# Kernel tuning notes

Measured on AMD Instinct MI355X. Metric: run time of the kernel, lower is better.

The kernel has to match this reference:

```python
import jax, jax.numpy as jnp
import numpy as np
import math

B, M, H, K, SPAN = 8, 1024, 512, 8, 1024
D = H // K
MK = M + SPAN


def _skew(X, pad_value):
    # shift every row one step to the right: [N, M, L] -> [N, M, M+L]
    N, m, L = X.shape
    X = jnp.pad(X, ((0, 0), (0, 0), (0, m + 1)), constant_values=pad_value)
    X = X.reshape(N, -1)[:, :-m]
    return X.reshape(N, m, m + L)


def _unskew(X):
    # reverse of _skew: [N, M, M+L] -> [N, M, L]
    N, m, Lk = X.shape
    L = Lk - m
    X = jnp.pad(X.reshape(N, -1), ((0, 0), (0, m)))
    return X.reshape(N, m, Lk + 1)[:, :, :L]


def setup_inputs() -> dict:
    key0 = jax.random.key(0)
    ks = jax.random.split(key0, 8)
    w_scale = 1.0 / math.sqrt(H)
    return {
        "query": jax.random.normal(ks[0], (B, M, H), jnp.float32),
        "key": jax.random.normal(ks[1], (B, MK, H), jnp.float32),
        "value": jax.random.normal(ks[2], (B, MK, H), jnp.float32),
        "pos_encoding": jax.random.normal(ks[3], (D, SPAN), jnp.float32) * w_scale,
        "Wq": jax.random.normal(ks[4], (H, H), jnp.float32) * w_scale,
        "Wk": jax.random.normal(ks[5], (H, H), jnp.float32) * w_scale,
        "Wv": jax.random.normal(ks[6], (H, H), jnp.float32) * w_scale,
        "Wo": jax.random.normal(ks[7], (H, H), jnp.float32) * w_scale,
    }


def _heads(x, W):
    # project then split heads: [B, T, H] -> [B*K, T, D]
    x = x @ W
    Bx, T, _ = x.shape
    x = x.reshape(Bx, T, K, D).transpose(0, 2, 1, 3)
    return x.reshape(Bx * K, T, D)


def reference(query, key, value, pos_encoding, Wq, Wk, Wv, Wo):
    q = _heads(query, Wq)      # [B*K, M, D]
    k = _heads(key, Wk)        # [B*K, MK, D]
    v = _heads(value, Wv)      # [B*K, MK, D]

    attn_ctx = jnp.einsum("nmd,nld->nml", q, k)   # [B*K, M, MK]
    attn_ctx = _unskew(attn_ctx)                    # [B*K, M, SPAN]
    attn_pos = jnp.einsum("nmd,ds->nms", q, pos_encoding)  # [B*K, M, SPAN]
    attn = jax.nn.softmax((attn_ctx + attn_pos) / math.sqrt(D), axis=-1)

    attn_sk = _skew(attn, 0.0)                      # [B*K, M, MK]
    out = jnp.einsum("nml,nld->nmd", attn_sk, v)   # [B*K, M, D]
    out = out.reshape(B, K, M, D).transpose(0, 2, 1, 3).reshape(B, M, H)
    return out @ Wo
```

## Files before the change

### kernel.cpp

```cpp
#include <hip/hip_runtime.h>
#include <stdint.h>

#define Bq 8
#define Mq 1024
#define Hq 512
#define NHq 8
#define Dq 64
#define SPANq 1024
#define MKq 2048
#define PR2 168

typedef __bf16 bf16x8 __attribute__((ext_vector_type(8)));
typedef _Float16 f16x8 __attribute__((ext_vector_type(8)));
typedef float f32x4 __attribute__((ext_vector_type(4)));
typedef unsigned short ushort8 __attribute__((ext_vector_type(8)));
typedef unsigned int uint2v __attribute__((ext_vector_type(2)));

static __device__ __forceinline__ unsigned short f2bf(float f) {
  union { float f; unsigned u; } x; x.f = f;
  unsigned r = x.u + 0x7FFFu + ((x.u >> 16) & 1u);
  return (unsigned short)(r >> 16);
}

static __device__ __forceinline__ unsigned pk_f16(float a, float b) {
  return __builtin_bit_cast(unsigned, __builtin_amdgcn_cvt_pkrtz(a, b));
}

static __device__ __forceinline__ f32x4 mfma_bf16(bf16x8 a, bf16x8 b, f32x4 c) {
  return __builtin_amdgcn_mfma_f32_16x16x32_bf16(a, b, c, 0, 0, 0);
}
static __device__ __forceinline__ f32x4 mfma_f16(f16x8 a, f16x8 b, f32x4 c) {
  return __builtin_amdgcn_mfma_f32_16x16x32_f16(a, b, c, 0, 0, 0);
}

static __device__ __forceinline__ void async_ld16(const void* g, void* l) {
  __builtin_amdgcn_global_load_lds(
      (const __attribute__((address_space(1))) void*)g,
      (__attribute__((address_space(3))) void*)l, 16, 0, 0);
}

__global__ __launch_bounds__(256) void conv_bf16(
    const float* __restrict__ q, const float* __restrict__ k,
    const float* __restrict__ v, unsigned short* __restrict__ qo,
    unsigned short* __restrict__ ko, unsigned short* __restrict__ vo) {
  const int z = blockIdx.y;
  const float* src = (z == 0) ? q : (z == 1) ? k : v;
  unsigned short* dst = (z == 0) ? qo : (z == 1) ? ko : vo;
  const int n = (z == 0) ? (Bq * Mq * Hq) : (Bq * MKq * Hq);
  const int idx = (blockIdx.x * 256 + threadIdx.x) * 8;
  if (idx >= n) return;
  const f32x4 f0 = *(const f32x4*)(src + idx);
  const f32x4 f1 = *(const f32x4*)(src + idx + 4);
  ushort8 h;
  h[0] = f2bf(f0[0]); h[1] = f2bf(f0[1]); h[2] = f2bf(f0[2]); h[3] = f2bf(f0[3]);
  h[4] = f2bf(f1[0]); h[5] = f2bf(f1[1]); h[6] = f2bf(f1[2]); h[7] = f2bf(f1[3]);
  *(ushort8*)(dst + idx) = h;
}

__global__ __launch_bounds__(256) void prep_transpose(
    const float* __restrict__ Wq, const float* __restrict__ Wk,
    const float* __restrict__ Wv, const float* __restrict__ Wo,
    const float* __restrict__ pos,
    unsigned short* __restrict__ WTq, unsigned short* __restrict__ WTk,
    unsigned short* __restrict__ WTv, unsigned short* __restrict__ WTo,
    unsigned short* __restrict__ posT) {
  __shared__ float tile[64][65];
  const int bid = blockIdx.x;
  const float* src; unsigned short* dst;
  int src_stride, dst_stride, i0, o0;
  if (bid < 256) {
    const int w = bid >> 6, t = bid & 63;
    src = (w == 0) ? Wq : (w == 1) ? Wk : (w == 2) ? Wv : Wo;
    dst = (w == 0) ? WTq : (w == 1) ? WTk : (w == 2) ? WTv : WTo;
    src_stride = Hq; dst_stride = Hq;
    i0 = (t >> 3) * 64; o0 = (t & 7) * 64;
  } else {
    const int t = bid - 256;
    src = pos; dst = posT;
    src_stride = SPANq; dst_stride = Dq;
    i0 = 0; o0 = t * 64;
  }
  const int tid = threadIdx.x;
  for (int e = tid; e < 4096; e += 256) {
    const int r = e >> 6, c = e & 63;
    tile[r][c] = src[(size_t)(i0 + r) * src_stride + o0 + c];
  }
  __syncthreads();
  for (int e = tid; e < 4096; e += 256) {
    const int r = e >> 6, c = e & 63;
    dst[(size_t)(o0 + r) * dst_stride + i0 + c] = f2bf(tile[c][r]);
  }
}

__global__ __launch_bounds__(256, 2) void gemm128(
    const unsigned short* __restrict__ Xb, const unsigned short* __restrict__ WT,
    unsigned short* __restrict__ outb, _Float16* __restrict__ outv,
    float* __restrict__ outf, int mode, int tshift) {
  __shared__ unsigned short sh[18432];
  unsigned short* As = sh;
  unsigned short* Bs = sh + 8192;
  const int tid = threadIdx.x;
  const int wave = tid >> 6, lane = tid & 63;
  const int q = lane >> 4, l16 = lane & 15;
  const int wy = wave >> 1, wx = wave & 1;
  const size_t m0 = (size_t)blockIdx.x * 128;
  const int n0 = blockIdx.y * 128;
  const int dsub = lane >> 3;
  const int dswz = (lane & 7) ^ dsub;

  f32x4 acc[4][4] = {};

  for (int k0 = 0; k0 < Hq; k0 += 64) {
    __syncthreads();
#pragma unroll
    for (int i = 0; i < 4; i++) {
      const int s = wave * 4 + i;
      const int r = s * 8 + dsub;
      async_ld16(Xb + (m0 + r) * Hq + k0 + dswz * 8, As + s * 512);
      async_ld16(WT + (size_t)(n0 + r) * Hq + k0 + dswz * 8, Bs + s * 512);
    }
    __syncthreads();
    bf16x8 af[2][4], bg[2][4];
#pragma unroll
    for (int h = 0; h < 2; h++) {
#pragma unroll
      for (int mt = 0; mt < 4; mt++) {
        const int R = wy * 64 + mt * 16 + l16;
        af[h][mt] = *(const bf16x8*)(As + R * 64 + (((h * 4 + q) ^ (l16 & 7)) * 8));
      }
#pragma unroll
      for (int nt = 0; nt < 4; nt++) {
        const int R = wx * 64 + nt * 16 + l16;
        bg[h][nt] = *(const bf16x8*)(Bs + R * 64 + (((h * 4 + q) ^ (l16 & 7)) * 8));
      }
    }
#pragma unroll
    for (int h = 0; h < 2; h++)
#pragma unroll
      for (int mt = 0; mt < 4; mt++)
#pragma unroll
        for (int nt = 0; nt < 4; nt++)
          acc[mt][nt] = mfma_bf16(af[h][mt], bg[h][nt], acc[mt][nt]);
  }

  if (mode == 2) {
    __syncthreads();
    _Float16* tr = (_Float16*)sh + wave * 4608;
#pragma unroll
    for (int nt = 0; nt < 4; nt++)
#pragma unroll
      for (int mt = 0; mt < 4; mt++)
#pragma unroll
        for (int r = 0; r < 4; r++)
          tr[(nt * 16 + l16) * 72 + mt * 16 + q * 4 + r] = (_Float16)acc[mt][nt][r];
    const int head = blockIdx.y * 2 + wx;
    const int mrow0 = (int)m0 + wy * 64;
    const int Tlen = 1 << tshift;
    const int b = mrow0 >> tshift, t0 = mrow0 & (Tlen - 1);
#pragma unroll
    for (int it = 0; it < 8; it++) {
      const int dl = it * 8 + (lane >> 3), tl = (lane & 7) * 8;
      const f16x8 v = *(const f16x8*)(tr + dl * 72 + tl);
      *(f16x8*)(outv + ((size_t)((b * 8 + head) * 64 + dl)) * Tlen + t0 + tl) = v;
    }
    return;
  }

  const int Tlen = 1 << tshift;
#pragma unroll
  for (int mt = 0; mt < 4; mt++) {
#pragma unroll
    for (int nt = 0; nt < 4; nt++) {
      const int c = n0 + wx * 64 + nt * 16 + l16;
#pragma unroll
      for (int r = 0; r < 4; r++) {
        const int m = (int)m0 + wy * 64 + mt * 16 + q * 4 + r;
        const float val = acc[mt][nt][r];
        if (mode == 3) {
          outf[(size_t)m * Hq + c] = val;
        } else {
          const int b = m >> tshift, t = m & (Tlen - 1);
          const int head = c >> 6, d = c & 63;
          outb[(((size_t)(b * 8 + head) << tshift) + t) * 64 + d] = f2bf(val);
        }
      }
    }
  }
}

__global__ __launch_bounds__(256, 2) void attn3(
    const unsigned short* __restrict__ qb, const unsigned short* __restrict__ kglob,
    const _Float16* __restrict__ vT, const unsigned short* __restrict__ posT,
    unsigned short* __restrict__ ctx) {
  __shared__ unsigned short Kt[12288];
  __shared__ unsigned short Pt[8192];
  __shared__ unsigned short Psh[4 * 16 * PR2];

  const int tid = threadIdx.x;
  const int wave = tid >> 6, lane = tid & 63;
  const int q = lane >> 4, l16 = lane & 15;
  const int n = blockIdx.y;
  const int m0 = blockIdx.x * 64;
  const int m0w = m0 + wave * 16;
  const int dsub = lane >> 3;
  const int dswz = (lane & 7) ^ dsub;

  unsigned short* row = Psh + (wave * 16 + l16) * PR2;

  const unsigned short* qbase = qb + ((size_t)n * Mq + m0w + l16) * Dq;
  const bf16x8 qf0 = *(const bf16x8*)(qbase + q * 8);
  const bf16x8 qf1 = *(const bf16x8*)(qbase + 32 + q * 8);

  const unsigned short* kbn = kglob + (size_t)n * MKq * Dq;
  const _Float16* vbn = vT + (size_t)n * Dq * MKq;

  f32x4 O[4] = {};
  float zrow = 0.f, mrow = -1e30f;

  for (int c = 0; c < 8; c++) {
    const int sbase = c * 128;
    const int jb = m0 + sbase;
    const int j00 = m0w + sbase;

    __syncthreads();
#pragma unroll
    for (int i = 0; i < 6; i++) {
      const int s = wave + 4 * i;
      const int r = s * 8 + dsub;
      async_ld16(kbn + (size_t)(jb + r) * Dq + dswz * 8, Kt + s * 512);
    }
#pragma unroll
    for (int i = 0; i < 4; i++) {
      const int s = wave + 4 * i;
      const int r = s * 8 + dsub;
      async_ld16(posT + (size_t)(sbase + r) * Dq + dswz * 8, Pt + s * 512);
    }
    __syncthreads();

#pragma unroll
    for (int t = 0; t < 8; t++) {
      const int rl = t * 16 + l16;
      const int ch = (q ^ (l16 & 7)) * 8;
      const bf16x8 p0 = *(const bf16x8*)(Pt + rl * 64 + ch);
      const bf16x8 p1 = *(const bf16x8*)(Pt + rl * 64 + (ch ^ 32));
      f32x4 b = {};
      b = mfma_bf16(p0, qf0, b);
      b = mfma_bf16(p1, qf1, b);
      const int cw = 16 + t * 16 + 4 * q + l16;
      row[cw + 0] = f2bf(b[0]);
      row[cw + 1] = f2bf(b[1]);
      row[cw + 2] = f2bf(b[2]);
      row[cw + 3] = f2bf(b[3]);
    }

    f32x4 S[9];
#pragma unroll
    for (int t = 0; t < 9; t++) {
      const int rl = wave * 16 + t * 16 + l16;
      const int ch = (q ^ (l16 & 7)) * 8;
      const bf16x8 k0 = *(const bf16x8*)(Kt + rl * 64 + ch);
      const bf16x8 k1 = *(const bf16x8*)(Kt + rl * 64 + (ch ^ 32));
      f32x4 a = {};
      a = mfma_bf16(k0, qf0, a);
      a = mfma_bf16(k1, qf1, a);
      const uint2v pv = *(const uint2v*)(row + 16 + t * 16 + 4 * q);
      a[0] += __uint_as_float(pv.x << 16);
      a[1] += __uint_as_float(pv.x & 0xffff0000u);
      a[2] += __uint_as_float(pv.y << 16);
      a[3] += __uint_as_float(pv.y & 0xffff0000u);
      S[t] = a;
    }
#pragma unroll
    for (int r = 0; r < 4; r++) {
      if (4 * q + r < l16) S[0][r] = -1e30f;
      if (4 * q + r >= l16) S[8][r] = -1e30f;
    }

    float mx = -1e30f;
#pragma unroll
    for (int t = 0; t < 9; t++)
      mx = fmaxf(mx, fmaxf(fmaxf(S[t][0], S[t][1]), fmaxf(S[t][2], S[t][3])));
    mx = fmaxf(mx, __shfl_xor(mx, 16, 64));
    mx = fmaxf(mx, __shfl_xor(mx, 32, 64));
    const float m_new = fmaxf(mrow, mx);
    const float alpha = __expf((mrow - m_new) * 0.125f);
    float zs = 0.f;
#pragma unroll
    for (int t = 0; t < 9; t++) {
#pragma unroll
      for (int r = 0; r < 4; r++) {
        const float e = __expf((S[t][r] - m_new) * 0.125f);
        S[t][r] = e; zs += e;
      }
    }
    zs += __shfl_xor(zs, 16, 64);
    zs += __shfl_xor(zs, 32, 64);
    zrow = zrow * alpha + zs;
    mrow = m_new;
#pragma unroll
    for (int dt = 0; dt < 4; dt++) O[dt] *= alpha;

#pragma unroll
    for (int t = 0; t < 9; t++) {
      *(unsigned*)(row + t * 16 + 4 * q) = pk_f16(S[t][0], S[t][1]);
      *(unsigned*)(row + t * 16 + 4 * q + 2) = pk_f16(S[t][2], S[t][3]);
    }
    *(unsigned*)(row + 144 + 4 * q) = 0u;
    *(unsigned*)(row + 144 + 4 * q + 2) = 0u;

    f16x8 Bf[5];
#pragma unroll
    for (int kt = 0; kt < 5; kt++)
      Bf[kt] = *(const f16x8*)(row + kt * 32 + q * 8);
    f16x8 Vv[5][4];
#pragma unroll
    for (int kt = 0; kt < 5; kt++) {
      int j = j00 + kt * 32 + q * 8;
      if (j > MKq - 8) j = MKq - 8;
#pragma unroll
      for (int dt = 0; dt < 4; dt++)
        Vv[kt][dt] = *(const f16x8*)(vbn + (size_t)(dt * 16 + l16) * MKq + j);
    }
#pragma unroll
    for (int kt = 0; kt < 5; kt++)
#pragma unroll
      for (int dt = 0; dt < 4; dt++)
        O[dt] = mfma_f16(Vv[kt][dt], Bf[kt], O[dt]);
  }

  const float zi = 1.f / zrow;
  unsigned short* cp = ctx + ((size_t)(n >> 3) * Mq + m0w + l16) * Hq + (n & 7) * Dq;
#pragma unroll
  for (int dt = 0; dt < 4; dt++)
#pragma unroll
    for (int r = 0; r < 4; r++)
      cp[dt * 16 + q * 4 + r] = f2bf(O[dt][r] * zi);
}

extern "C" void kernel_launch(void* const* d_in, const int* in_sizes, int n_in,
                              void* d_out, int out_size, void* d_ws, size_t ws_size,
                              hipStream_t stream) {
  const float* query = (const float*)d_in[0];
  const float* key   = (const float*)d_in[1];
  const float* value = (const float*)d_in[2];
  const float* pos   = (const float*)d_in[3];
  const float* Wq    = (const float*)d_in[4];
  const float* Wk    = (const float*)d_in[5];
  const float* Wv    = (const float*)d_in[6];
  const float* Wo    = (const float*)d_in[7];
  float* out = (float*)d_out;

  char* w = (char*)d_ws;
  unsigned short* qX   = (unsigned short*)w; w += (size_t)Bq * Mq * Hq * 2;
  unsigned short* kX   = (unsigned short*)w; w += (size_t)Bq * MKq * Hq * 2;
  unsigned short* vX   = (unsigned short*)w; w += (size_t)Bq * MKq * Hq * 2;
  unsigned short* qb   = (unsigned short*)w; w += (size_t)64 * Mq * Dq * 2;
  unsigned short* kbuf = (unsigned short*)w; w += (size_t)64 * MKq * Dq * 2;
  _Float16*       vTb  = (_Float16*)w;       w += (size_t)64 * Dq * MKq * 2;
  unsigned short* posT = (unsigned short*)w; w += (size_t)SPANq * Dq * 2;
  unsigned short* WTq  = (unsigned short*)w; w += (size_t)Hq * Hq * 2;
  unsigned short* WTk  = (unsigned short*)w; w += (size_t)Hq * Hq * 2;
  unsigned short* WTv  = (unsigned short*)w; w += (size_t)Hq * Hq * 2;
  unsigned short* WTo  = (unsigned short*)w; w += (size_t)Hq * Hq * 2;
  unsigned short* ctx  = (unsigned short*)w; w += (size_t)Bq * Mq * Hq * 2;

  prep_transpose<<<272, 256, 0, stream>>>(Wq, Wk, Wv, Wo, pos, WTq, WTk, WTv, WTo, posT);
  conv_bf16<<<dim3(4096, 3), 256, 0, stream>>>(query, key, value, qX, kX, vX);
  gemm128<<<dim3(64, 4), 256, 0, stream>>>(qX, WTq, qb, nullptr, nullptr, 0, 10);
  gemm128<<<dim3(128, 4), 256, 0, stream>>>(kX, WTk, kbuf, nullptr, nullptr, 0, 11);
  gemm128<<<dim3(128, 4), 256, 0, stream>>>(vX, WTv, nullptr, vTb, nullptr, 2, 11);
  attn3<<<dim3(16, 64), 256, 0, stream>>>(qb, kbuf, vTb, posT, ctx);
  gemm128<<<dim3(64, 4), 256, 0, stream>>>(ctx, WTo, nullptr, nullptr, out, 3, 10);
}
```

Baseline: 286.9 us.

## Merge prep and QKV GEMM launches, pipeline K tiles in attention

Folds the weight/pos transpose and the bf16 input conversion into one launch, and merges the Q, K and V projections into a single grid. This cuts launch count and lets small grids fill the device together. The attention kernel now prefetches the next K tile and computes the next positional-bias row before the softmax and PV work of the current chunk. It reads pos directly from global memory instead of staging it in LDS, and remaps block IDs so heads interleave across CUs. GEMM launch bounds rise to 4 waves per SIMD and fragment loads are split per k-half to cut register pressure, at the cost of extra barriers and a different block-to-data mapping.

After: 321.2 us. 1.12x slower.

```diff
diff --git a/kernel.cpp b/kernel.cpp
--- a/kernel.cpp
+++ b/kernel.cpp
@@ -39,33 +39,35 @@
       (__attribute__((address_space(3))) void*)l, 16, 0, 0);
 }
 
-__global__ __launch_bounds__(256) void conv_bf16(
-    const float* __restrict__ q, const float* __restrict__ k,
-    const float* __restrict__ v, unsigned short* __restrict__ qo,
-    unsigned short* __restrict__ ko, unsigned short* __restrict__ vo) {
-  const int z = blockIdx.y;
-  const float* src = (z == 0) ? q : (z == 1) ? k : v;
-  unsigned short* dst = (z == 0) ? qo : (z == 1) ? ko : vo;
-  const int n = (z == 0) ? (Bq * Mq * Hq) : (Bq * MKq * Hq);
-  const int idx = (blockIdx.x * 256 + threadIdx.x) * 8;
-  if (idx >= n) return;
-  const f32x4 f0 = *(const f32x4*)(src + idx);
-  const f32x4 f1 = *(const f32x4*)(src + idx + 4);
-  ushort8 h;
-  h[0] = f2bf(f0[0]); h[1] = f2bf(f0[1]); h[2] = f2bf(f0[2]); h[3] = f2bf(f0[3]);
-  h[4] = f2bf(f1[0]); h[5] = f2bf(f1[1]); h[6] = f2bf(f1[2]); h[7] = f2bf(f1[3]);
-  *(ushort8*)(dst + idx) = h;
-}
-
-__global__ __launch_bounds__(256) void prep_transpose(
+__global__ __launch_bounds__(256) void prep_all(
+    const float* __restrict__ query, const float* __restrict__ key,
+    const float* __restrict__ value,
     const float* __restrict__ Wq, const float* __restrict__ Wk,
     const float* __restrict__ Wv, const float* __restrict__ Wo,
     const float* __restrict__ pos,
+    unsigned short* __restrict__ qX, unsigned short* __restrict__ kX,
+    unsigned short* __restrict__ vX,
     unsigned short* __restrict__ WTq, unsigned short* __restrict__ WTk,
     unsigned short* __restrict__ WTv, unsigned short* __restrict__ WTo,
     unsigned short* __restrict__ posT) {
   __shared__ float tile[64][65];
   const int bid = blockIdx.x;
+  const int tid = threadIdx.x;
+  if (bid >= 272) {
+    const int rem = bid - 272;
+    const float* src; unsigned short* dst; int off;
+    if (rem < 2048)      { src = query; dst = qX; off = rem; }
+    else if (rem < 6144) { src = key;   dst = kX; off = rem - 2048; }
+    else                 { src = value; dst = vX; off = rem - 6144; }
+    const int idx = off * 2048 + tid * 8;
+    const f32x4 f0 = *(const f32x4*)(src + idx);
+    const f32x4 f1 = *(const f32x4*)(src + idx + 4);
+    ushort8 h;
+    h[0] = f2bf(f0[0]); h[1] = f2bf(f0[1]); h[2] = f2bf(f0[2]); h[3] = f2bf(f0[3]);
+    h[4] = f2bf(f1[0]); h[5] = f2bf(f1[1]); h[6] = f2bf(f1[2]); h[7] = f2bf(f1[3]);
+    *(ushort8*)(dst + idx) = h;
+    return;
+  }
   const float* src; unsigned short* dst;
   int src_stride, dst_stride, i0, o0;
   if (bid < 256) {
@@ -80,7 +82,6 @@
     src_stride = SPANq; dst_stride = Dq;
     i0 = 0; o0 = t * 64;
   }
-  const int tid = threadIdx.x;
   for (int e = tid; e < 4096; e += 256) {
     const int r = e >> 6, c = e & 63;
     tile[r][c] = src[(size_t)(i0 + r) * src_stride + o0 + c];
@@ -92,19 +93,19 @@
   }
 }
 
-__global__ __launch_bounds__(256, 2) void gemm128(
+static __device__ __forceinline__ void gemm_body(
     const unsigned short* __restrict__ Xb, const unsigned short* __restrict__ WT,
     unsigned short* __restrict__ outb, _Float16* __restrict__ outv,
-    float* __restrict__ outf, int mode, int tshift) {
-  __shared__ unsigned short sh[18432];
+    float* __restrict__ outf, int mode, int tshift, int bx, int by,
+    unsigned short* sh) {
   unsigned short* As = sh;
   unsigned short* Bs = sh + 8192;
   const int tid = threadIdx.x;
   const int wave = tid >> 6, lane = tid & 63;
   const int q = lane >> 4, l16 = lane & 15;
   const int wy = wave >> 1, wx = wave & 1;
-  const size_t m0 = (size_t)blockIdx.x * 128;
-  const int n0 = blockIdx.y * 128;
+  const size_t m0 = (size_t)bx * 128;
+  const int n0 = by * 128;
   const int dsub = lane >> 3;
   const int dswz = (lane & 7) ^ dsub;
 
@@ -120,27 +121,25 @@
       async_ld16(WT + (size_t)(n0 + r) * Hq + k0 + dswz * 8, Bs + s * 512);
     }
     __syncthreads();
-    bf16x8 af[2][4], bg[2][4];
 #pragma unroll
     for (int h = 0; h < 2; h++) {
+      bf16x8 af[4], bg[4];
 #pragma unroll
       for (int mt = 0; mt < 4; mt++) {
         const int R = wy * 64 + mt * 16 + l16;
-        af[h][mt] = *(const bf16x8*)(As + R * 64 + (((h * 4 + q) ^ (l16 & 7)) * 8));
+        af[mt] = *(const bf16x8*)(As + R * 64 + (((h * 4 + q) ^ (l16 & 7)) * 8));
       }
 #pragma unroll
       for (int nt = 0; nt < 4; nt++) {
         const int R = wx * 64 + nt * 16 + l16;
-        bg[h][nt] = *(const bf16x8*)(Bs + R * 64 + (((h * 4 + q) ^ (l16 & 7)) * 8));
-      }
-    }
-#pragma unroll
-    for (int h = 0; h < 2; h++)
+        bg[nt] = *(const bf16x8*)(Bs + R * 64 + (((h * 4 + q) ^ (l16 & 7)) * 8));
+      }
 #pragma unroll
       for (int mt = 0; mt < 4; mt++)
 #pragma unroll
         for (int nt = 0; nt < 4; nt++)
-          acc[mt][nt] = mfma_bf16(af[h][mt], bg[h][nt], acc[mt][nt]);
+          acc[mt][nt] = mfma_bf16(af[mt], bg[nt], acc[mt][nt]);
+    }
   }
 
   if (mode == 2) {
@@ -153,7 +152,7 @@
 #pragma unroll
         for (int r = 0; r < 4; r++)
           tr[(nt * 16 + l16) * 72 + mt * 16 + q * 4 + r] = (_Float16)acc[mt][nt][r];
-    const int head = blockIdx.y * 2 + wx;
+    const int head = by * 2 + wx;
     const int mrow0 = (int)m0 + wy * 64;
     const int Tlen = 1 << tshift;
     const int b = mrow0 >> tshift, t0 = mrow0 & (Tlen - 1);
@@ -188,24 +187,55 @@
   }
 }
 
-__global__ __launch_bounds__(256, 2) void attn3(
+__global__ __launch_bounds__(256, 4) void gemm_qkv(
+    const unsigned short* __restrict__ qX, const unsigned short* __restrict__ kX,
+    const unsigned short* __restrict__ vX,
+    const unsigned short* __restrict__ WTq, const unsigned short* __restrict__ WTk,
+    const unsigned short* __restrict__ WTv,
+    unsigned short* __restrict__ qb, unsigned short* __restrict__ kbuf,
+    _Float16* __restrict__ vTb) {
+  __shared__ unsigned short sh[18432];
+  const int bid = blockIdx.x;
+  if (bid < 256) {
+    gemm_body(qX, WTq, qb, nullptr, nullptr, 0, 10, bid & 63, bid >> 6, sh);
+  } else if (bid < 768) {
+    const int b2 = bid - 256;
+    gemm_body(kX, WTk, kbuf, nullptr, nullptr, 0, 11, b2 & 127, b2 >> 7, sh);
+  } else {
+    const int b2 = bid - 768;
+    gemm_body(vX, WTv, nullptr, vTb, nullptr, 2, 11, b2 & 127, b2 >> 7, sh);
+  }
+}
+
+__global__ __launch_bounds__(256, 4) void gemm_out(
+    const unsigned short* __restrict__ ctx, const unsigned short* __restrict__ WTo,
+    float* __restrict__ out) {
+  __shared__ unsigned short sh[18432];
+  const int bid = blockIdx.x;
+  gemm_body(ctx, WTo, nullptr, nullptr, out, 3, 10, bid & 63, bid >> 6, sh);
+}
+
+__global__ __launch_bounds__(256, 2) void attn4(
     const unsigned short* __restrict__ qb, const unsigned short* __restrict__ kglob,
     const _Float16* __restrict__ vT, const unsigned short* __restrict__ posT,
     unsigned short* __restrict__ ctx) {
   __shared__ unsigned short Kt[12288];
-  __shared__ unsigned short Pt[8192];
-  __shared__ unsigned short Psh[4 * 16 * PR2];
+  __shared__ unsigned short PosR[4 * 16 * PR2];
+  __shared__ unsigned short Prow[4 * 16 * PR2];
 
   const int tid = threadIdx.x;
   const int wave = tid >> 6, lane = tid & 63;
   const int q = lane >> 4, l16 = lane & 15;
-  const int n = blockIdx.y;
-  const int m0 = blockIdx.x * 64;
+  const int bid = blockIdx.x;
+  const int n = (bid & 7) * 8 + (bid >> 7);
+  const int mtile = (bid >> 3) & 15;
+  const int m0 = mtile * 64;
   const int m0w = m0 + wave * 16;
   const int dsub = lane >> 3;
   const int dswz = (lane & 7) ^ dsub;
 
-  unsigned short* row = Psh + (wave * 16 + l16) * PR2;
+  unsigned short* prow = Prow + (wave * 16 + l16) * PR2;
+  unsigned short* posr = PosR + (wave * 16 + l16) * PR2;
 
   const unsigned short* qbase = qb + ((size_t)n * Mq + m0w + l16) * Dq;
   const bf16x8 qf0 = *(const bf16x8*)(qbase + q * 8);
@@ -217,41 +247,36 @@
   f32x4 O[4] = {};
   float zrow = 0.f, mrow = -1e30f;
 
+#pragma unroll
+  for (int i = 0; i < 6; i++) {
+    const int s = wave + 4 * i;
+    const int r = s * 8 + dsub;
+    async_ld16(kbn + (size_t)(m0 + r) * Dq + dswz * 8, Kt + s * 512);
+  }
+  {
+    bf16x8 pf[8][2];
+#pragma unroll
+    for (int t = 0; t < 8; t++) {
+      const unsigned short* pp = posT + (size_t)(t * 16 + l16) * Dq + q * 8;
+      pf[t][0] = *(const bf16x8*)pp;
+      pf[t][1] = *(const bf16x8*)(pp + 32);
+    }
+#pragma unroll
+    for (int t = 0; t < 8; t++) {
+      f32x4 b = {};
+      b = mfma_bf16(pf[t][0], qf0, b);
+      b = mfma_bf16(pf[t][1], qf1, b);
+      const int cw = 16 + t * 16 + 4 * q + l16;
+      posr[cw + 0] = f2bf(b[0]);
+      posr[cw + 1] = f2bf(b[1]);
+      posr[cw + 2] = f2bf(b[2]);
+      posr[cw + 3] = f2bf(b[3]);
+    }
+  }
+  __syncthreads();
+
   for (int c = 0; c < 8; c++) {
-    const int sbase = c * 128;
-    const int jb = m0 + sbase;
-    const int j00 = m0w + sbase;
-
-    __syncthreads();
-#pragma unroll
-    for (int i = 0; i < 6; i++) {
-      const int s = wave + 4 * i;
-      const int r = s * 8 + dsub;
-      async_ld16(kbn + (size_t)(jb + r) * Dq + dswz * 8, Kt + s * 512);
-    }
-#pragma unroll
-    for (int i = 0; i < 4; i++) {
-      const int s = wave + 4 * i;
-      const int r = s * 8 + dsub;
-      async_ld16(posT + (size_t)(sbase + r) * Dq + dswz * 8, Pt + s * 512);
-    }
-    __syncthreads();
-
-#pragma unroll
-    for (int t = 0; t < 8; t++) {
-      const int rl = t * 16 + l16;
-      const int ch = (q ^ (l16 & 7)) * 8;
-      const bf16x8 p0 = *(const bf16x8*)(Pt + rl * 64 + ch);
-      const bf16x8 p1 = *(const bf16x8*)(Pt + rl * 64 + (ch ^ 32));
-      f32x4 b = {};
-      b = mfma_bf16(p0, qf0, b);
-      b = mfma_bf16(p1, qf1, b);
-      const int cw = 16 + t * 16 + 4 * q + l16;
-      row[cw + 0] = f2bf(b[0]);
-      row[cw + 1] = f2bf(b[1]);
-      row[cw + 2] = f2bf(b[2]);
-      row[cw + 3] = f2bf(b[3]);
-    }
+    const int j00 = m0w + c * 128;
 
     f32x4 S[9];
 #pragma unroll
@@ -263,7 +288,7 @@
       f32x4 a = {};
       a = mfma_bf16(k0, qf0, a);
       a = mfma_bf16(k1, qf1, a);
-      const uint2v pv = *(const uint2v*)(row + 16 + t * 16 + 4 * q);
+      const uint2v pv = *(const uint2v*)(posr + 16 + t * 16 + 4 * q);
       a[0] += __uint_as_float(pv.x << 16);
       a[1] += __uint_as_float(pv.x & 0xffff0000u);
       a[2] += __uint_as_float(pv.y << 16);
@@ -274,6 +299,36 @@
     for (int r = 0; r < 4; r++) {
       if (4 * q + r < l16) S[0][r] = -1e30f;
       if (4 * q + r >= l16) S[8][r] = -1e30f;
+    }
+
+    if (c < 7) {
+      __syncthreads();
+      const int jb1 = m0 + (c + 1) * 128;
+#pragma unroll
+      for (int i = 0; i < 6; i++) {
+        const int s = wave + 4 * i;
+        const int r = s * 8 + dsub;
+        async_ld16(kbn + (size_t)(jb1 + r) * Dq + dswz * 8, Kt + s * 512);
+      }
+      const int sb1 = (c + 1) * 128;
+      bf16x8 pf[8][2];
+#pragma unroll
+      for (int t = 0; t < 8; t++) {
+        const unsigned short* pp = posT + (size_t)(sb1 + t * 16 + l16) * Dq + q * 8;
+        pf[t][0] = *(const bf16x8*)pp;
+        pf[t][1] = *(const bf16x8*)(pp + 32);
+      }
+#pragma unroll
+      for (int t = 0; t < 8; t++) {
+        f32x4 b = {};
+        b = mfma_bf16(pf[t][0], qf0, b);
+        b = mfma_bf16(pf[t][1], qf1, b);
+        const int cw = 16 + t * 16 + 4 * q + l16;
+        posr[cw + 0] = f2bf(b[0]);
+        posr[cw + 1] = f2bf(b[1]);
+        posr[cw + 2] = f2bf(b[2]);
+        posr[cw + 3] = f2bf(b[3]);
+      }
     }
 
     float mx = -1e30f;
@@ -302,16 +357,16 @@
 
 #pragma unroll
     for (int t = 0; t < 9; t++) {
-      *(unsigned*)(row + t * 16 + 4 * q) = pk_f16(S[t][0], S[t][1]);
-      *(unsigned*)(row + t * 16 + 4 * q + 2) = pk_f16(S[t][2], S[t][3]);
-    }
-    *(unsigned*)(row + 144 + 4 * q) = 0u;
-    *(unsigned*)(row + 144 + 4 * q + 2) = 0u;
+      *(unsigned*)(prow + t * 16 + 4 * q) = pk_f16(S[t][0], S[t][1]);
+      *(unsigned*)(prow + t * 16 + 4 * q + 2) = pk_f16(S[t][2], S[t][3]);
+    }
+    *(unsigned*)(prow + 144 + 4 * q) = 0u;
+    *(unsigned*)(prow + 144 + 4 * q + 2) = 0u;
 
     f16x8 Bf[5];
 #pragma unroll
     for (int kt = 0; kt < 5; kt++)
-      Bf[kt] = *(const f16x8*)(row + kt * 32 + q * 8);
+      Bf[kt] = *(const f16x8*)(prow + kt * 32 + q * 8);
     f16x8 Vv[5][4];
 #pragma unroll
     for (int kt = 0; kt < 5; kt++) {
@@ -326,6 +381,8 @@
 #pragma unroll
       for (int dt = 0; dt < 4; dt++)
         O[dt] = mfma_f16(Vv[kt][dt], Bf[kt], O[dt]);
+
+    if (c < 7) __syncthreads();
   }
 
   const float zi = 1.f / zrow;
@@ -364,11 +421,9 @@
   unsigned short* WTo  = (unsigned short*)w; w += (size_t)Hq * Hq * 2;
   unsigned short* ctx  = (unsigned short*)w; w += (size_t)Bq * Mq * Hq * 2;
 
-  prep_transpose<<<272, 256, 0, stream>>>(Wq, Wk, Wv, Wo, pos, WTq, WTk, WTv, WTo, posT);
-  conv_bf16<<<dim3(4096, 3), 256, 0, stream>>>(query, key, value, qX, kX, vX);
-  gemm128<<<dim3(64, 4), 256, 0, stream>>>(qX, WTq, qb, nullptr, nullptr, 0, 10);
-  gemm128<<<dim3(128, 4), 256, 0, stream>>>(kX, WTk, kbuf, nullptr, nullptr, 0, 11);
-  gemm128<<<dim3(128, 4), 256, 0, stream>>>(vX, WTv, nullptr, vTb, nullptr, 2, 11);
-  attn3<<<dim3(16, 64), 256, 0, stream>>>(qb, kbuf, vTb, posT, ctx);
-  gemm128<<<dim3(64, 4), 256, 0, stream>>>(ctx, WTo, nullptr, nullptr, out, 3, 10);
-}
+  prep_all<<<10512, 256, 0, stream>>>(query, key, value, Wq, Wk, Wv, Wo, pos,
+                                      qX, kX, vX, WTq, WTk, WTv, WTo, posT);
+  gemm_qkv<<<1280, 256, 0, stream>>>(qX, kX, vX, WTq, WTk, WTv, qb, kbuf, vTb);
+  attn4<<<1024, 256, 0, stream>>>(qb, kbuf, vTb, posT, ctx);
+  gemm_out<<<256, 256, 0, stream>>>(ctx, WTo, out);
+}
```
